# Kernel optimization log

Hardware: AMD Instinct MI355X
Metric: run time of the kernel (lower is better)

## Reference

```python
import jax, jax.numpy as jnp
import numpy as np

B = 1024      # batch
E = 1024      # encoding_dim
OUT = 34      # 17 joints x 2 coords


def setup_inputs() -> dict:
    key = jax.random.key(0)
    ks = jax.random.split(key, 8)
    s = 0.02  # weight init scale
    return {
        "h": jax.random.normal(ks[0], (B, E), dtype=jnp.float32),
        "c": jax.random.normal(ks[1], (B, E), dtype=jnp.float32),
        "W_ih": jax.random.normal(ks[2], (4 * E, E), dtype=jnp.float32) * s,
        "W_hh": jax.random.normal(ks[3], (4 * E, E), dtype=jnp.float32) * s,
        "b_ih": jax.random.normal(ks[4], (4 * E,), dtype=jnp.float32) * s,
        "b_hh": jax.random.normal(ks[5], (4 * E,), dtype=jnp.float32) * s,
        "W_out": jax.random.normal(ks[6], (OUT, E), dtype=jnp.float32) * s,
        "b_out": jax.random.normal(ks[7], (OUT,), dtype=jnp.float32) * s,
        "future_preds": 10,
    }


def reference(h, c, W_ih, W_hh, b_ih, b_hh, W_out, b_out, future_preds):
    E_ = h.shape[1]
    start = jnp.zeros_like(h)  # zeros=True start token

    def step(carry, _):
        h_t, c_t, x = carry
        # LSTMCell: gates in PyTorch order i, f, g, o
        gates = x @ W_ih.T + b_ih + h_t @ W_hh.T + b_hh  # [B, 4E]
        i = jax.nn.sigmoid(gates[:, 0 * E_:1 * E_])
        f = jax.nn.sigmoid(gates[:, 1 * E_:2 * E_])
        g = jnp.tanh(gates[:, 2 * E_:3 * E_])
        o = jax.nn.sigmoid(gates[:, 3 * E_:4 * E_])
        c_new = f * c_t + i * g
        h_new = o * jnp.tanh(c_new)
        return (h_new, c_new, h_new), h_new

    _, hs = jax.lax.scan(step, (h, c, start), None, length=future_preds)
    # hs: [T, B, E] -> [B, T, E]
    preds = jnp.transpose(hs, (1, 0, 2))
    return preds @ W_out.T + b_out  # [B, T, 34]
```

## Files before the change

### kernel.cpp

```cpp
#include <hip/hip_runtime.h>
#include <cstdint>
#include <cstddef>

#define E_DIM   1024
#define B_DIM   1024
#define T_STEPS 10
#define OUT_DIM 34
#define OUT_PAD 48
#define HSTR    24
#define QK      256
#define WQ_ELEMS (64 * QK)
#define DYN_LDS (2 * WQ_ELEMS * 2 + 128 * HSTR * 2)

typedef __attribute__((ext_vector_type(4))) float  f32x4;
typedef __attribute__((ext_vector_type(8))) __bf16 bf16x8;

__device__ __forceinline__ unsigned short f2bf(float f) {
    unsigned int u = __float_as_uint(f);
    u = (u + 0x7FFFu + ((u >> 16) & 1u)) >> 16;
    return (unsigned short)u;
}
__device__ __forceinline__ float sigmoid_(float x) { return 1.0f / (1.0f + __expf(-x)); }
__device__ __forceinline__ float tanh_(float x)    { return 2.0f / (1.0f + __expf(-2.0f * x)) - 1.0f; }

__global__ void prep_weights_frag(const float* __restrict__ W_ih, const float* __restrict__ W_hh,
                                  unsigned short* __restrict__ WsumF, unsigned short* __restrict__ WhhF) {
    const int bn = blockIdx.x >> 3, qtr = (blockIdx.x >> 1) & 3, half = blockIdx.x & 1;
    const int nt = threadIdx.x >> 6, lane = threadIdx.x & 63;
    const int j = lane & 15, q = lane >> 4;
    const int srow = nt * E_DIM + bn * 16 + j;
    const float* wi = W_ih + (size_t)srow * E_DIM;
    const float* wh = W_hh + (size_t)srow * E_DIM;
    const size_t dstb = (size_t)bn * 65536 + (size_t)qtr * 16384 + nt * 512 + lane * 8;
#pragma unroll
    for (int ks8i = 0; ks8i < 4; ++ks8i) {
        const int ks8 = half * 4 + ks8i;
        const int k = qtr * 256 + ks8 * 32 + q * 8;
        float4 i0 = *(const float4*)(wi + k);
        float4 i1 = *(const float4*)(wi + k + 4);
        float4 h0 = *(const float4*)(wh + k);
        float4 h1 = *(const float4*)(wh + k + 4);
        unsigned short* ds = WsumF + dstb + ks8 * 2048;
        unsigned short* dh = WhhF  + dstb + ks8 * 2048;
        ds[0] = f2bf(i0.x + h0.x); ds[1] = f2bf(i0.y + h0.y);
        ds[2] = f2bf(i0.z + h0.z); ds[3] = f2bf(i0.w + h0.w);
        ds[4] = f2bf(i1.x + h1.x); ds[5] = f2bf(i1.y + h1.y);
        ds[6] = f2bf(i1.z + h1.z); ds[7] = f2bf(i1.w + h1.w);
        dh[0] = f2bf(h0.x); dh[1] = f2bf(h0.y); dh[2] = f2bf(h0.z); dh[3] = f2bf(h0.w);
        dh[4] = f2bf(h1.x); dh[5] = f2bf(h1.y); dh[6] = f2bf(h1.z); dh[7] = f2bf(h1.w);
    }
}

__global__ void prep_state(const float* __restrict__ h0, const float* __restrict__ c0,
                           const float* __restrict__ W_out,
                           const float* __restrict__ b_ih, const float* __restrict__ b_hh,
                           unsigned short* __restrict__ hbuf, unsigned short* __restrict__ Woutp,
                           float* __restrict__ bperm, float* __restrict__ C) {
    const int b = blockIdx.x;
    const int t = threadIdx.x;
    if (b < 1024) {
        const size_t i = ((size_t)b * 256 + t) * 4;
        float4 hv = *(const float4*)(h0 + i);
        hbuf[i + 0] = f2bf(hv.x);
        hbuf[i + 1] = f2bf(hv.y);
        hbuf[i + 2] = f2bf(hv.z);
        hbuf[i + 3] = f2bf(hv.w);
    } else if (b < 1072) {
        const int o = b - 1024;
        const int k = t * 4;
        float4 w = make_float4(0.f, 0.f, 0.f, 0.f);
        if (o < OUT_DIM) w = *(const float4*)(W_out + (size_t)o * E_DIM + k);
        const size_t dst = (size_t)o * E_DIM + k;
        Woutp[dst + 0] = f2bf(w.x);
        Woutp[dst + 1] = f2bf(w.y);
        Woutp[dst + 2] = f2bf(w.z);
        Woutp[dst + 3] = f2bf(w.w);
    } else if (b < 1088) {
        const int n = (b - 1072) * 256 + t;
        const int g = (n >> 4) & 3;
        const int e = ((n >> 6) << 4) | (n & 15);
        const int srow = g * E_DIM + e;
        bperm[n] = b_ih[srow] + b_hh[srow];
    } else {
        const int m = b - 1088;
        const int e0 = t * 4;
        float4 v = *(const float4*)(c0 + (size_t)m * E_DIM + e0);
        const int bm = m >> 7, wave = (m >> 5) & 3, mt = (m >> 4) & 1, q = (m >> 2) & 3, r = m & 3;
        const float vv[4] = {v.x, v.y, v.z, v.w};
#pragma unroll
        for (int ii = 0; ii < 4; ++ii) {
            const int e = e0 + ii;
            const int bn = e >> 4, jj = e & 15;
            const int lane = q * 16 + jj;
            C[(((size_t)(bn * 8 + bm) * 4 + wave) * 64 + lane) * 8 + mt * 4 + r] = vv[ii];
        }
    }
}

__global__ __launch_bounds__(256, 2) void lstm_step(
    const unsigned short* __restrict__ WF,
    const float* __restrict__ bp,
    const unsigned short* __restrict__ Hin,
    float* __restrict__ C,
    unsigned short* __restrict__ Hout)
{
    extern __shared__ __align__(16) unsigned short smem[];
    unsigned short* Wbuf0 = smem;
    unsigned short* Wbuf1 = smem + WQ_ELEMS;
    unsigned short* Ht    = smem + 2 * WQ_ELEMS;

    const int tid  = threadIdx.x;
    const int wave = tid >> 6;
    const int lane = tid & 63;
    const int bn = blockIdx.x;
    const int bm = blockIdx.y;
    const int j  = lane & 15;
    const int q  = lane >> 4;

    f32x4 acc[2][4];
#pragma unroll
    for (int a = 0; a < 2; ++a)
#pragma unroll
        for (int b = 0; b < 4; ++b) acc[a][b] = (f32x4){0.f, 0.f, 0.f, 0.f};

    const int nb = bn * 64 + j;
    const float bi = bp[nb +  0];
    const float bf = bp[nb + 16];
    const float bg = bp[nb + 32];
    const float bo = bp[nb + 48];
    const size_t cbase = (((size_t)(bn * 8 + bm) * 4 + wave) * 64 + lane) * 8;
    float4 cold0 = *(const float4*)(C + cbase);
    float4 cold1 = *(const float4*)(C + cbase + 4);

    const unsigned short* arow0 = Hin + (size_t)(bm * 128 + wave * 32 + j) * E_DIM + q * 8;
    const unsigned short* arow1 = arow0 + (size_t)16 * E_DIM;
    const unsigned short* wsrc  = WF + (size_t)bn * 65536;

    uint4 ra[8][2];
#pragma unroll
    for (int p = 0; p < 8; ++p) {
        ra[p][0] = *(const uint4*)(arow0 + p * 32);
        ra[p][1] = *(const uint4*)(arow1 + p * 32);
    }

    uint4 wreg[8];
#pragma unroll
    for (int i = 0; i < 8; ++i)
        wreg[i] = *(const uint4*)(wsrc + (i * 256 + tid) * 8);
#pragma unroll
    for (int i = 0; i < 8; ++i)
        *(uint4*)(Wbuf0 + (i * 256 + tid) * 8) = wreg[i];
    __syncthreads();

    for (int qtr = 0; qtr < 4; ++qtr) {
        if (qtr < 3) {
#pragma unroll
            for (int i = 0; i < 8; ++i)
                wreg[i] = *(const uint4*)(wsrc + (size_t)(qtr + 1) * WQ_ELEMS + (i * 256 + tid) * 8);
        }
        const unsigned short* wb = ((qtr & 1) ? Wbuf1 : Wbuf0) + lane * 8;
#pragma unroll
        for (int ks8 = 0; ks8 < 8; ++ks8) {
            const int ks = qtr * 8 + ks8;
            bf16x8 av0 = __builtin_bit_cast(bf16x8, ra[ks8][0]);
            bf16x8 av1 = __builtin_bit_cast(bf16x8, ra[ks8][1]);
            bf16x8 bv[4];
#pragma unroll
            for (int nt = 0; nt < 4; ++nt)
                bv[nt] = *(const bf16x8*)(wb + (ks8 * 4 + nt) * 512);
#pragma unroll
            for (int nt = 0; nt < 4; ++nt) {
                acc[0][nt] = __builtin_amdgcn_mfma_f32_16x16x32_bf16(av0, bv[nt], acc[0][nt], 0, 0, 0);
                acc[1][nt] = __builtin_amdgcn_mfma_f32_16x16x32_bf16(av1, bv[nt], acc[1][nt], 0, 0, 0);
            }
            if (ks < 24) {
                ra[ks8][0] = *(const uint4*)(arow0 + (ks + 8) * 32);
                ra[ks8][1] = *(const uint4*)(arow1 + (ks + 8) * 32);
            }
        }
        if (qtr < 3) {
            unsigned short* wn_ = ((qtr + 1) & 1) ? Wbuf1 : Wbuf0;
#pragma unroll
            for (int i = 0; i < 8; ++i)
                *(uint4*)(wn_ + (i * 256 + tid) * 8) = wreg[i];
            __syncthreads();
        }
    }

    float4 cnew[2];
    const float coldv[2][4] = {{cold0.x, cold0.y, cold0.z, cold0.w},
                               {cold1.x, cold1.y, cold1.z, cold1.w}};
#pragma unroll
    for (int mt = 0; mt < 2; ++mt) {
#pragma unroll
        for (int r = 0; r < 4; ++r) {
            const float iv = sigmoid_(acc[mt][0][r] + bi);
            const float fv = sigmoid_(acc[mt][1][r] + bf);
            const float gv = tanh_(acc[mt][2][r] + bg);
            const float ov = sigmoid_(acc[mt][3][r] + bo);
            const float cn = fv * coldv[mt][r] + iv * gv;
            cnew[mt][r] = cn;
            const int rowl = wave * 32 + mt * 16 + q * 4 + r;
            Ht[rowl * HSTR + j] = f2bf(ov * tanh_(cn));
        }
    }
    *(float4*)(C + cbase)     = cnew[0];
    *(float4*)(C + cbase + 4) = cnew[1];
    __syncthreads();

    {
        const int row = tid >> 1, part = tid & 1;
        uint4 v = *(const uint4*)(Ht + row * HSTR + part * 8);
        *(uint4*)(Hout + (size_t)(bm * 128 + row) * E_DIM + bn * 16 + part * 8) = v;
    }
}

__global__ __launch_bounds__(256) void proj_kernel(
    const unsigned short* __restrict__ Hs,
    const unsigned short* __restrict__ Wo,
    const float* __restrict__ b_out,
    float* __restrict__ Out)
{
    __shared__ float red[4][32][OUT_PAD];

    const int tid = threadIdx.x, wave = tid >> 6, lane = tid & 63;
    const int j = lane & 15, q = lane >> 4;
    const int t  = blockIdx.y;
    const int bb = blockIdx.x;
    const unsigned short* Hbase = Hs + ((size_t)t * B_DIM + (size_t)bb * 32) * E_DIM;
    const int k0 = wave * 256;

    f32x4 acc[2][3];
#pragma unroll
    for (int a = 0; a < 2; ++a)
#pragma unroll
        for (int b = 0; b < 3; ++b) acc[a][b] = (f32x4){0.f, 0.f, 0.f, 0.f};

#pragma unroll
    for (int kk = 0; kk < 256; kk += 32) {
        const int kc = k0 + kk + q * 8;
        bf16x8 av[2], bv[3];
#pragma unroll
        for (int mt = 0; mt < 2; ++mt)
            av[mt] = *(const bf16x8*)(Hbase + (size_t)(mt * 16 + j) * E_DIM + kc);
#pragma unroll
        for (int nt = 0; nt < 3; ++nt)
            bv[nt] = *(const bf16x8*)(Wo + (size_t)(nt * 16 + j) * E_DIM + kc);
#pragma unroll
        for (int mt = 0; mt < 2; ++mt)
#pragma unroll
            for (int nt = 0; nt < 3; ++nt)
                acc[mt][nt] = __builtin_amdgcn_mfma_f32_16x16x32_bf16(av[mt], bv[nt], acc[mt][nt], 0, 0, 0);
    }

#pragma unroll
    for (int mt = 0; mt < 2; ++mt)
#pragma unroll
        for (int nt = 0; nt < 3; ++nt)
#pragma unroll
            for (int r = 0; r < 4; ++r)
                red[wave][mt * 16 + q * 4 + r][nt * 16 + j] = acc[mt][nt][r];
    __syncthreads();

#pragma unroll
    for (int ii = 0; ii < 6; ++ii) {
        const int idx = tid * 6 + ii;
        const int row = idx / OUT_PAD, o = idx % OUT_PAD;
        if (o < OUT_DIM) {
            const float s = red[0][row][o] + red[1][row][o] + red[2][row][o] + red[3][row][o];
            Out[((size_t)(bb * 32 + row) * T_STEPS + t) * OUT_DIM + o] = s + b_out[o];
        }
    }
}

extern "C" void kernel_launch(void* const* d_in, const int* in_sizes, int n_in,
                              void* d_out, int out_size, void* d_ws, size_t ws_size,
                              hipStream_t stream) {
    (void)in_sizes; (void)n_in; (void)out_size; (void)ws_size;
    const float* h     = (const float*)d_in[0];
    const float* c     = (const float*)d_in[1];
    const float* W_ih  = (const float*)d_in[2];
    const float* W_hh  = (const float*)d_in[3];
    const float* b_ih  = (const float*)d_in[4];
    const float* b_hh  = (const float*)d_in[5];
    const float* W_out = (const float*)d_in[6];
    const float* b_out = (const float*)d_in[7];
    float* out = (float*)d_out;

    char* ws = (char*)d_ws;
    unsigned short* WsumF = (unsigned short*)(ws + 0);
    unsigned short* WhhF  = (unsigned short*)(ws + 8388608);
    float*          bperm = (float*)(ws + 16777216);
    unsigned short* Woutp = (unsigned short*)(ws + 16842752);
    float*          cbuf  = (float*)(ws + 16941056);
    unsigned short* hs    = (unsigned short*)(ws + 21135360);

    hipFuncSetAttribute((const void*)lstm_step,
                        hipFuncAttributeMaxDynamicSharedMemorySize, DYN_LDS);

    prep_weights_frag<<<512, 256, 0, stream>>>(W_ih, W_hh, WsumF, WhhF);
    prep_state<<<2112, 256, 0, stream>>>(h, c, W_out, b_ih, b_hh, hs, Woutp, bperm, cbuf);

    lstm_step<<<dim3(64, 8), 256, DYN_LDS, stream>>>(WhhF, bperm, hs, cbuf,
                                                     hs + (size_t)B_DIM * E_DIM);
    for (int t = 1; t < T_STEPS; ++t)
        lstm_step<<<dim3(64, 8), 256, DYN_LDS, stream>>>(WsumF, bperm,
                                                         hs + (size_t)t * B_DIM * E_DIM,
                                                         cbuf,
                                                         hs + (size_t)(t + 1) * B_DIM * E_DIM);

    proj_kernel<<<dim3(32, T_STEPS), 256, 0, stream>>>(hs + (size_t)B_DIM * E_DIM,
                                                       Woutp, b_out, out);
}
```

Before: 327.6 us.

## Halve LSTM step block M-tile to 64 rows and double grid for occupancy

Each lstm_step block now covers 64 batch rows instead of 128. Each wave computes one 16-row M tile instead of two, and weights are staged in eighth-K chunks with a smaller LDS double buffer. The grid doubles to 64x16 blocks and launch bounds ask for 4 blocks per CU, which cuts register and LDS use so more blocks run at once and the 256-CU machine is better filled. In exchange each weight fragment in LDS is reused by half as many rows, so global weight traffic per step doubles, and there are more barriers per block.

```diff
diff --git a/kernel.cpp b/kernel.cpp
--- a/kernel.cpp
+++ b/kernel.cpp
@@ -8,9 +8,8 @@
 #define OUT_DIM 34
 #define OUT_PAD 48
 #define HSTR    24
-#define QK      256
-#define WQ_ELEMS (64 * QK)
-#define DYN_LDS (2 * WQ_ELEMS * 2 + 128 * HSTR * 2)
+#define WE_ELEMS (64 * 128)
+#define DYN_LDS (2 * WE_ELEMS * 2 + 64 * HSTR * 2)
 
 typedef __attribute__((ext_vector_type(4))) float  f32x4;
 typedef __attribute__((ext_vector_type(8))) __bf16 bf16x8;
@@ -97,7 +96,7 @@
     }
 }
 
-__global__ __launch_bounds__(256, 2) void lstm_step(
+__global__ __launch_bounds__(256, 4) void lstm_step(
     const unsigned short* __restrict__ WF,
     const float* __restrict__ bp,
     const unsigned short* __restrict__ Hin,
@@ -106,112 +105,97 @@
 {
     extern __shared__ __align__(16) unsigned short smem[];
     unsigned short* Wbuf0 = smem;
-    unsigned short* Wbuf1 = smem + WQ_ELEMS;
-    unsigned short* Ht    = smem + 2 * WQ_ELEMS;
+    unsigned short* Wbuf1 = smem + WE_ELEMS;
+    unsigned short* Ht    = smem + 2 * WE_ELEMS;
 
     const int tid  = threadIdx.x;
-    const int wave = tid >> 6;
+    const int w    = tid >> 6;
     const int lane = tid & 63;
     const int bn = blockIdx.x;
-    const int bm = blockIdx.y;
+    const int g  = blockIdx.y;
     const int j  = lane & 15;
     const int q  = lane >> 4;
 
-    f32x4 acc[2][4];
-#pragma unroll
-    for (int a = 0; a < 2; ++a)
-#pragma unroll
-        for (int b = 0; b < 4; ++b) acc[a][b] = (f32x4){0.f, 0.f, 0.f, 0.f};
+    f32x4 acc[4];
+#pragma unroll
+    for (int b = 0; b < 4; ++b) acc[b] = (f32x4){0.f, 0.f, 0.f, 0.f};
 
     const int nb = bn * 64 + j;
     const float bi = bp[nb +  0];
     const float bf = bp[nb + 16];
     const float bg = bp[nb + 32];
     const float bo = bp[nb + 48];
-    const size_t cbase = (((size_t)(bn * 8 + bm) * 4 + wave) * 64 + lane) * 8;
-    float4 cold0 = *(const float4*)(C + cbase);
-    float4 cold1 = *(const float4*)(C + cbase + 4);
-
-    const unsigned short* arow0 = Hin + (size_t)(bm * 128 + wave * 32 + j) * E_DIM + q * 8;
-    const unsigned short* arow1 = arow0 + (size_t)16 * E_DIM;
-    const unsigned short* wsrc  = WF + (size_t)bn * 65536;
-
-    uint4 ra[8][2];
-#pragma unroll
-    for (int p = 0; p < 8; ++p) {
-        ra[p][0] = *(const uint4*)(arow0 + p * 32);
-        ra[p][1] = *(const uint4*)(arow1 + p * 32);
-    }
-
-    uint4 wreg[8];
-#pragma unroll
-    for (int i = 0; i < 8; ++i)
+    const size_t cbase = (((size_t)(bn * 8 + (g >> 1)) * 4 + ((g & 1) * 2 + (w >> 1))) * 64 + lane) * 8
+                         + (size_t)(w & 1) * 4;
+    float4 cold = *(const float4*)(C + cbase);
+
+    const unsigned short* arow = Hin + (size_t)(g * 64 + w * 16 + j) * E_DIM + q * 8;
+    const unsigned short* wsrc = WF + (size_t)bn * 65536;
+
+    uint4 ra[8];
+#pragma unroll
+    for (int p = 0; p < 8; ++p)
+        ra[p] = *(const uint4*)(arow + p * 32);
+
+    uint4 wreg[4];
+#pragma unroll
+    for (int i = 0; i < 4; ++i)
         wreg[i] = *(const uint4*)(wsrc + (i * 256 + tid) * 8);
 #pragma unroll
-    for (int i = 0; i < 8; ++i)
+    for (int i = 0; i < 4; ++i)
         *(uint4*)(Wbuf0 + (i * 256 + tid) * 8) = wreg[i];
     __syncthreads();
 
-    for (int qtr = 0; qtr < 4; ++qtr) {
-        if (qtr < 3) {
-#pragma unroll
-            for (int i = 0; i < 8; ++i)
-                wreg[i] = *(const uint4*)(wsrc + (size_t)(qtr + 1) * WQ_ELEMS + (i * 256 + tid) * 8);
-        }
-        const unsigned short* wb = ((qtr & 1) ? Wbuf1 : Wbuf0) + lane * 8;
-#pragma unroll
-        for (int ks8 = 0; ks8 < 8; ++ks8) {
-            const int ks = qtr * 8 + ks8;
-            bf16x8 av0 = __builtin_bit_cast(bf16x8, ra[ks8][0]);
-            bf16x8 av1 = __builtin_bit_cast(bf16x8, ra[ks8][1]);
+    for (int e = 0; e < 8; ++e) {
+        if (e < 7) {
+#pragma unroll
+            for (int i = 0; i < 4; ++i)
+                wreg[i] = *(const uint4*)(wsrc + (size_t)(e + 1) * WE_ELEMS + (i * 256 + tid) * 8);
+        }
+        const unsigned short* wb = ((e & 1) ? Wbuf1 : Wbuf0) + lane * 8;
+#pragma unroll
+        for (int ks8l = 0; ks8l < 4; ++ks8l) {
+            const int ks = e * 4 + ks8l;
+            bf16x8 av = __builtin_bit_cast(bf16x8, ra[ks & 7]);
             bf16x8 bv[4];
 #pragma unroll
             for (int nt = 0; nt < 4; ++nt)
-                bv[nt] = *(const bf16x8*)(wb + (ks8 * 4 + nt) * 512);
-#pragma unroll
-            for (int nt = 0; nt < 4; ++nt) {
-                acc[0][nt] = __builtin_amdgcn_mfma_f32_16x16x32_bf16(av0, bv[nt], acc[0][nt], 0, 0, 0);
-                acc[1][nt] = __builtin_amdgcn_mfma_f32_16x16x32_bf16(av1, bv[nt], acc[1][nt], 0, 0, 0);
-            }
-            if (ks < 24) {
-                ra[ks8][0] = *(const uint4*)(arow0 + (ks + 8) * 32);
-                ra[ks8][1] = *(const uint4*)(arow1 + (ks + 8) * 32);
-            }
-        }
-        if (qtr < 3) {
-            unsigned short* wn_ = ((qtr + 1) & 1) ? Wbuf1 : Wbuf0;
-#pragma unroll
-            for (int i = 0; i < 8; ++i)
+                bv[nt] = *(const bf16x8*)(wb + (ks8l * 4 + nt) * 512);
+#pragma unroll
+            for (int nt = 0; nt < 4; ++nt)
+                acc[nt] = __builtin_amdgcn_mfma_f32_16x16x32_bf16(av, bv[nt], acc[nt], 0, 0, 0);
+            if (ks < 24)
+                ra[ks & 7] = *(const uint4*)(arow + (ks + 8) * 32);
+        }
+        if (e < 7) {
+            unsigned short* wn_ = ((e + 1) & 1) ? Wbuf1 : Wbuf0;
+#pragma unroll
+            for (int i = 0; i < 4; ++i)
                 *(uint4*)(wn_ + (i * 256 + tid) * 8) = wreg[i];
             __syncthreads();
         }
     }
 
-    float4 cnew[2];
-    const float coldv[2][4] = {{cold0.x, cold0.y, cold0.z, cold0.w},
-                               {cold1.x, cold1.y, cold1.z, cold1.w}};
-#pragma unroll
-    for (int mt = 0; mt < 2; ++mt) {
-#pragma unroll
-        for (int r = 0; r < 4; ++r) {
-            const float iv = sigmoid_(acc[mt][0][r] + bi);
-            const float fv = sigmoid_(acc[mt][1][r] + bf);
-            const float gv = tanh_(acc[mt][2][r] + bg);
-            const float ov = sigmoid_(acc[mt][3][r] + bo);
-            const float cn = fv * coldv[mt][r] + iv * gv;
-            cnew[mt][r] = cn;
-            const int rowl = wave * 32 + mt * 16 + q * 4 + r;
-            Ht[rowl * HSTR + j] = f2bf(ov * tanh_(cn));
-        }
-    }
-    *(float4*)(C + cbase)     = cnew[0];
-    *(float4*)(C + cbase + 4) = cnew[1];
+    float4 cnew;
+    const float coldv[4] = {cold.x, cold.y, cold.z, cold.w};
+#pragma unroll
+    for (int r = 0; r < 4; ++r) {
+        const float iv = sigmoid_(acc[0][r] + bi);
+        const float fv = sigmoid_(acc[1][r] + bf);
+        const float gv = tanh_(acc[2][r] + bg);
+        const float ov = sigmoid_(acc[3][r] + bo);
+        const float cn = fv * coldv[r] + iv * gv;
+        cnew[r] = cn;
+        const int rowl = w * 16 + q * 4 + r;
+        Ht[rowl * HSTR + j] = f2bf(ov * tanh_(cn));
+    }
+    *(float4*)(C + cbase) = cnew;
     __syncthreads();
 
-    {
+    if (tid < 128) {
         const int row = tid >> 1, part = tid & 1;
         uint4 v = *(const uint4*)(Ht + row * HSTR + part * 8);
-        *(uint4*)(Hout + (size_t)(bm * 128 + row) * E_DIM + bn * 16 + part * 8) = v;
+        *(uint4*)(Hout + (size_t)(g * 64 + row) * E_DIM + bn * 16 + part * 8) = v;
     }
 }
 
@@ -301,13 +285,13 @@
     prep_weights_frag<<<512, 256, 0, stream>>>(W_ih, W_hh, WsumF, WhhF);
     prep_state<<<2112, 256, 0, stream>>>(h, c, W_out, b_ih, b_hh, hs, Woutp, bperm, cbuf);
 
-    lstm_step<<<dim3(64, 8), 256, DYN_LDS, stream>>>(WhhF, bperm, hs, cbuf,
-                                                     hs + (size_t)B_DIM * E_DIM);
+    lstm_step<<<dim3(64, 16), 256, DYN_LDS, stream>>>(WhhF, bperm, hs, cbuf,
+                                                      hs + (size_t)B_DIM * E_DIM);
     for (int t = 1; t < T_STEPS; ++t)
-        lstm_step<<<dim3(64, 8), 256, DYN_LDS, stream>>>(WsumF, bperm,
-                                                         hs + (size_t)t * B_DIM * E_DIM,
-                                                         cbuf,
-                                                         hs + (size_t)(t + 1) * B_DIM * E_DIM);
+        lstm_step<<<dim3(64, 16), 256, DYN_LDS, stream>>>(WsumF, bperm,
+                                                          hs + (size_t)t * B_DIM * E_DIM,
+                                                          cbuf,
+                                                          hs + (size_t)(t + 1) * B_DIM * E_DIM);
 
     proj_kernel<<<dim3(32, T_STEPS), 256, 0, stream>>>(hs + (size_t)B_DIM * E_DIM,
                                                        Woutp, b_out, out);
```

Result: slower. 339.3 us (+3.6%).
